# Performance work log

Measured on AMD Instinct MI355X. Metric: run time of the kernel, lower is better.

The kernel has to match this reference:

```python
import jax, jax.numpy as jnp
import numpy as np

N_MET = 100_000
N_RXN = 50_000
E_SUB = 2_000_000
E_ALL = 4_000_000
MSG_DIM = 16
HIDDEN = 32


def setup_inputs() -> dict:
    key = jax.random.key(0)
    ks = jax.random.split(key, 16)
    x_met = jax.random.normal(ks[0], (N_MET,), dtype=jnp.float32)
    sto_sub = jax.random.uniform(ks[1], (E_SUB,), dtype=jnp.float32, minval=0.0, maxval=1.0)
    sto_all = jax.random.normal(ks[2], (E_ALL,), dtype=jnp.float32)
    met_sub = jax.random.randint(ks[3], (E_SUB,), 0, N_MET)
    rxn_sub = jax.random.randint(ks[4], (E_SUB,), 0, N_RXN)
    met_all = jax.random.randint(ks[5], (E_ALL,), 0, N_MET)
    rxn_all = jax.random.randint(ks[6], (E_ALL,), 0, N_RXN)
    # msg_mlp: Linear(2->HIDDEN), Tanh, Linear(HIDDEN->MSG_DIM)
    W1m = jax.random.normal(ks[7], (2, HIDDEN), jnp.float32) / np.sqrt(2.0)
    b1m = jnp.zeros((HIDDEN,), jnp.float32)
    W2m = jax.random.normal(ks[8], (HIDDEN, MSG_DIM), jnp.float32) / np.sqrt(HIDDEN)
    b2m = jnp.zeros((MSG_DIM,), jnp.float32)
    # rate_mlp: Linear(MSG_DIM->HIDDEN), Tanh, Linear(HIDDEN->1)
    W1r = jax.random.normal(ks[9], (MSG_DIM, HIDDEN), jnp.float32) / np.sqrt(MSG_DIM)
    b1r = jnp.zeros((HIDDEN,), jnp.float32)
    W2r = jax.random.normal(ks[10], (HIDDEN, 1), jnp.float32) / np.sqrt(HIDDEN)
    b2r = jnp.zeros((1,), jnp.float32)
    return {
        "x_met": x_met, "sto_sub": sto_sub, "sto_all": sto_all,
        "W1m": W1m, "b1m": b1m, "W2m": W2m, "b2m": b2m,
        "W1r": W1r, "b1r": b1r, "W2r": W2r, "b2r": b2r,
        "met_sub": met_sub, "rxn_sub": rxn_sub,
        "met_all": met_all, "rxn_all": rxn_all,
    }


def reference(x_met, sto_sub, sto_all, W1m, b1m, W2m, b2m, W1r, b1r, W2r, b2r,
              met_sub, rxn_sub, met_all, rxn_all):
    # gather substrate node features and build per-edge MLP input [E_sub, 2]
    msg_in = jnp.stack([x_met[met_sub], sto_sub], axis=-1)
    # msg MLP: tanh hidden, linear out -> [E_sub, MSG_DIM]
    msg = jnp.tanh(msg_in @ W1m + b1m) @ W2m + b2m
    # scatter-add messages into reactions -> [N_RXN, MSG_DIM]
    h_rxn = jax.ops.segment_sum(msg, rxn_sub, num_segments=N_RXN)
    # rate MLP + softplus -> per-reaction rate v [N_RXN]
    v = jax.nn.softplus((jnp.tanh(h_rxn @ W1r + b1r) @ W2r + b2r)[:, 0])
    # stoichiometric contributions scattered into metabolites -> dxdt [N_MET]
    contrib = sto_all * v[rxn_all]
    dxdt = jax.ops.segment_sum(contrib, met_all, num_segments=N_MET)
    return dxdt, v
```

## Files before the change

### kernel.cpp

```cpp
#include <hip/hip_runtime.h>

#define N_MET 100000
#define N_RXN 50000
#define E_SUB 2000000
#define E_ALL 4000000
#define MSG_DIM 16
#define HIDDEN 32

#define NBKT_A 391
#define NB_ALL 245
#define TILE_A 16384
#define LOFFA_W (NBKT_A + 1)
#define NBKT_S 782
#define NB_SUB 245
#define TILE_S 8192


__device__ __forceinline__ float fast_tanh(float x) {
    const float ax = fabsf(x);
    const float e = __expf(2.0f * ax);
    const float t = 1.0f - 2.0f * __builtin_amdgcn_rcpf(e + 1.0f);
    return copysignf(t, x);
}


__global__ __launch_bounds__(1024) void hist_sub_kernel(
    const int* __restrict__ rxn_sub, int* __restrict__ histS)
{
    __shared__ int hb[NBKT_S];
    const int t = threadIdx.x, bk = blockIdx.x;
    for (int i = t; i < NBKT_S; i += 1024) hb[i] = 0;
    __syncthreads();
#pragma unroll
    for (int k = 0; k < 2; ++k) {
        const int i = bk * 2048 + (k << 10) + t;
        if (i < E_SUB / 4) {
            const int4 r = ((const int4*)rxn_sub)[i];
            atomicAdd(&hb[r.x >> 6], 1);
            atomicAdd(&hb[r.y >> 6], 1);
            atomicAdd(&hb[r.z >> 6], 1);
            atomicAdd(&hb[r.w >> 6], 1);
        }
    }
    __syncthreads();
    for (int i = t; i < NBKT_S; i += 1024) histS[bk * NBKT_S + i] = hb[i];
}

__global__ __launch_bounds__(256) void scan_cols_sub_kernel(
    int* __restrict__ histS, int* __restrict__ tot_s)
{
    __shared__ int wsum[4];
    const int b = blockIdx.x;
    const int t = threadIdx.x, lane = t & 63, w = t >> 6;
    const int val = (t < NB_SUB) ? histS[(size_t)t * NBKT_S + b] : 0;
    int x = val;
#pragma unroll
    for (int off = 1; off < 64; off <<= 1) {
        const int y = __shfl_up(x, off);
        if (lane >= off) x += y;
    }
    if (lane == 63) wsum[w] = x;
    __syncthreads();
    if (w == 0) {
        int s = (lane < 4) ? wsum[lane] : 0;
#pragma unroll
        for (int off = 1; off < 4; off <<= 1) {
            const int y = __shfl_up(s, off);
            if (lane >= off) s += y;
        }
        if (lane < 4) wsum[lane] = s;
    }
    __syncthreads();
    const int excl = ((w > 0) ? wsum[w - 1] : 0) + x - val;
    if (t < NB_SUB) histS[(size_t)t * NBKT_S + b] = excl;
    if (t == 0) tot_s[b] = wsum[3];
}

__global__ __launch_bounds__(256) void scan_base_sub_kernel(
    const int* __restrict__ tot_s, int* __restrict__ base_s)
{
    __shared__ int wsum[4];
    const int t = threadIdx.x, lane = t & 63, w = t >> 6;
    int carry = 0;
    for (int basei = 0; basei < NBKT_S; basei += 256) {
        const int i = basei + t;
        const int val = (i < NBKT_S) ? tot_s[i] : 0;
        int x = val;
#pragma unroll
        for (int off = 1; off < 64; off <<= 1) {
            const int y = __shfl_up(x, off);
            if (lane >= off) x += y;
        }
        if (lane == 63) wsum[w] = x;
        __syncthreads();
        if (w == 0) {
            int s = (lane < 4) ? wsum[lane] : 0;
#pragma unroll
            for (int off = 1; off < 4; off <<= 1) {
                const int y = __shfl_up(s, off);
                if (lane >= off) s += y;
            }
            if (lane < 4) wsum[lane] = s;
        }
        __syncthreads();
        const int excl = carry + ((w > 0) ? wsum[w - 1] : 0) + x - val;
        if (i < NBKT_S) base_s[i] = excl;
        carry += wsum[3];
        __syncthreads();
    }
}


__global__ __launch_bounds__(1024) void scatter_bin_sub_kernel(
    const float* __restrict__ x_met, const float* __restrict__ sto_sub,
    const int* __restrict__ met_sub, const int* __restrict__ rxn_sub,
    const int* __restrict__ hist, const int* __restrict__ base,
    float2* __restrict__ pxs)
{
    __shared__ float2 se[TILE_S];
    __shared__ int cnt[NBKT_S];
    __shared__ int loff[NBKT_S + 1];
    __shared__ int goff[NBKT_S];
    const int t = threadIdx.x, bk = blockIdx.x;
    for (int i = t; i < NBKT_S; i += 1024) {
        cnt[i] = 0;
        goff[i] = hist[bk * NBKT_S + i] + base[i];
    }
    __syncthreads();

    const int e0 = bk * TILE_S;
    const int rem = min(TILE_S, E_SUB - e0);
    const int tb = 8 * t;
    float2 pay[8]; int meta[8];
    if (tb + 8 <= rem) {
        const int4 r01 = ((const int4*)(rxn_sub + e0))[2 * t];
        const int4 r23 = ((const int4*)(rxn_sub + e0))[2 * t + 1];
        const int4 m01 = ((const int4*)(met_sub + e0))[2 * t];
        const int4 m23 = ((const int4*)(met_sub + e0))[2 * t + 1];
        const float4 s01 = ((const float4*)(sto_sub + e0))[2 * t];
        const float4 s23 = ((const float4*)(sto_sub + e0))[2 * t + 1];
        const int rr[8] = {r01.x, r01.y, r01.z, r01.w, r23.x, r23.y, r23.z, r23.w};
        const int mm[8] = {m01.x, m01.y, m01.z, m01.w, m23.x, m23.y, m23.z, m23.w};
        const float ss[8] = {s01.x, s01.y, s01.z, s01.w, s23.x, s23.y, s23.z, s23.w};
#pragma unroll
        for (int k = 0; k < 8; ++k) {
            const int r = rr[k];
            const float x = x_met[mm[k]];
            const int sb = (__float_as_int(ss[k]) & ~63) | (r & 63);
            pay[k] = make_float2(x, __int_as_float(sb));
            const int q = r >> 6;
            meta[k] = (atomicAdd(&cnt[q], 1) << 10) | q;
        }
    } else {
#pragma unroll
        for (int k = 0; k < 8; ++k) {
            const int e = e0 + tb + k;
            if (e < E_SUB) {
                const int r = rxn_sub[e];
                const float x = x_met[met_sub[e]];
                const int sb = (__float_as_int(sto_sub[e]) & ~63) | (r & 63);
                pay[k] = make_float2(x, __int_as_float(sb));
                const int q = r >> 6;
                meta[k] = (atomicAdd(&cnt[q], 1) << 10) | q;
            } else meta[k] = -1;
        }
    }
    __syncthreads();

    if (t < 64) {
        int carry = 0;
        for (int bb = 0; bb < NBKT_S; bb += 64) {
            const int idx = bb + t;
            const int val = (idx < NBKT_S) ? cnt[idx] : 0;
            int x = val;
#pragma unroll
            for (int off = 1; off < 64; off <<= 1) {
                const int y = __shfl_up(x, off);
                if (t >= off) x += y;
            }
            if (idx < NBKT_S) loff[idx] = carry + x - val;
            carry += __shfl(x, 63);
        }
        if (t == 0) loff[NBKT_S] = carry;
    }
    __syncthreads();

#pragma unroll
    for (int k = 0; k < 8; ++k) {
        if (meta[k] >= 0)
            se[loff[meta[k] & 1023] + (meta[k] >> 10)] = pay[k];
    }
    __syncthreads();

    const int w = t >> 6, lane = t & 63;
    for (int q = w; q < NBKT_S; q += 16) {
        const int s = loff[q], lenq = loff[q + 1] - s, d = goff[q];
        for (int i = lane; i < lenq; i += 64)
            pxs[d + i] = se[s + i];
    }
}

__global__ __launch_bounds__(512, 6) void bucket_msg_kernel(
    const float2* __restrict__ pxs,
    const int* __restrict__ base, const int* __restrict__ tot,
    const float* __restrict__ W1m, const float* __restrict__ b1m,
    const float* __restrict__ W2m, const float* __restrict__ b2m,
    const float* __restrict__ W1r, const float* __restrict__ b1r,
    const float* __restrict__ W2r, const float* __restrict__ b2r,
    float* __restrict__ v)
{
    __shared__ float2 se[4096];
    __shared__ float  sth[64 * 33];
    __shared__ int    cnt[64];
    __shared__ int    soff[65];
    __shared__ int    ccnt[64];
    __shared__ float  sW2m[HIDDEN * MSG_DIM];
    __shared__ float  sb2m[MSG_DIM];
    __shared__ float  sW1r[MSG_DIM * HIDDEN];
    __shared__ float  sb1r[HIDDEN];
    __shared__ float  sW2r[HIDDEN];
    __shared__ float  sb2r;
    __shared__ float  sh[64 * 17];

    const int t = threadIdx.x;
    const int w = t >> 6, l = t & 63;
    const int half = l >> 5, j = l & 31;

    for (int i = t; i < HIDDEN * MSG_DIM; i += 512) sW2m[i] = W2m[i];
    for (int i = t; i < MSG_DIM * HIDDEN; i += 512) sW1r[i] = W1r[i];
    if (t < MSG_DIM) sb2m[t] = b2m[t];
    if (t < HIDDEN) sb1r[t] = b1r[t];
    if (t >= 64 && t < 64 + HIDDEN) sW2r[t - 64] = W2r[t - 64];
    if (t == 128) sb2r = b2r[0];
    if (t < 64) ccnt[t] = 0;

    const float w1x = W1m[j];
    const float w1y = W1m[HIDDEN + j];
    const float w1b = b1m[j];

    const int b = blockIdx.x;
    const int beg = base[b];
    const int end = beg + tot[b];

    float acc[4] = {0.0f, 0.0f, 0.0f, 0.0f};

    for (int cb = beg; cb < end; cb += 4096) {
        if (t < 64) cnt[t] = 0;
        __syncthreads();

        float2 pay[8];
        int meta[8];
#pragma unroll
        for (int k = 0; k < 8; ++k) {
            const int idx = cb + t + (k << 9);
            if (idx < end) {
                const float2 pv = pxs[idx];
                const int r = __float_as_int(pv.y) & 63;
                meta[k] = (atomicAdd(&cnt[r], 1) << 6) | r;
                pay[k] = pv;
            } else meta[k] = -1;
        }
        __syncthreads();

        if (t < 64) {
            const int orig = cnt[t];
            int x = orig;
#pragma unroll
            for (int off = 1; off < 64; off <<= 1) {
                const int y = __shfl_up(x, off);
                if (t >= off) x += y;
            }
            soff[t] = x - orig;
            if (t == 63) soff[64] = x;
            ccnt[t] += orig;
        }
        __syncthreads();

#pragma unroll
        for (int k = 0; k < 8; ++k) {
            if (meta[k] >= 0)
                se[soff[meta[k] & 63] + (meta[k] >> 6)] = pay[k];
        }
        __syncthreads();

#pragma unroll
        for (int p = 0; p < 4; ++p) {
            const int q = (w << 3) + (p << 1) + half;
            const int rb = soff[q];
            const int rl = soff[q + 1] - rb;
            float a0 = 0.0f, a1 = 0.0f;
            int i = 0;
            for (; i + 2 <= rl; i += 2) {
                const float2 e0 = se[rb + i];
                const float2 e1 = se[rb + i + 1];
                a0 += fast_tanh(fmaf(e0.x, w1x, fmaf(e0.y, w1y, w1b)));
                a1 += fast_tanh(fmaf(e1.x, w1x, fmaf(e1.y, w1y, w1b)));
            }
            if (i < rl) {
                const float2 e0 = se[rb + i];
                a0 += fast_tanh(fmaf(e0.x, w1x, fmaf(e0.y, w1y, w1b)));
            }
            acc[p] += a0 + a1;
        }
        __syncthreads();
    }

#pragma unroll
    for (int p = 0; p < 4; ++p) {
        const int q = (w << 3) + (p << 1) + half;
        sth[q * 33 + j] = acc[p];
    }
    __syncthreads();

    {
        const int r = t & 63, g = (t >> 6) << 1;
        const float cntf = (float)ccnt[r];
        float h0 = cntf * sb2m[g + 0], h1 = cntf * sb2m[g + 1];
#pragma unroll 8
        for (int jj = 0; jj < HIDDEN; ++jj) {
            const float ts = sth[r * 33 + jj];
            h0 = fmaf(ts, sW2m[jj * MSG_DIM + g + 0], h0);
            h1 = fmaf(ts, sW2m[jj * MSG_DIM + g + 1], h1);
        }
        sh[r * 17 + g + 0] = h0;
        sh[r * 17 + g + 1] = h1;
    }
    __syncthreads();

    if (t < 64) {
        const int r = b * 64 + t;
        if (r < N_RXN) {
            float h[MSG_DIM];
#pragma unroll
            for (int d = 0; d < MSG_DIM; ++d) h[d] = sh[t * 17 + d];
            float acc2 = sb2r;
#pragma unroll 2
            for (int jj = 0; jj < HIDDEN; ++jj) {
                float z = sb1r[jj];
#pragma unroll
                for (int d = 0; d < MSG_DIM; ++d)
                    z = fmaf(h[d], sW1r[d * HIDDEN + jj], z);
                acc2 = fmaf(fast_tanh(z), sW2r[jj], acc2);
            }
            v[r] = fmaxf(acc2, 0.0f) + log1pf(expf(-fabsf(acc2)));
        }
    }
}


__global__ __launch_bounds__(1024) void scatter_bin_kernel(
    const float* __restrict__ sto_all, const float* __restrict__ v,
    const int* __restrict__ met_all, const int* __restrict__ rxn_all,
    int* __restrict__ loffA, float* __restrict__ pc)
{
    __shared__ float sp[TILE_A];
    __shared__ int cnt[NBKT_A];
    __shared__ int loff[NBKT_A + 1];
    const int t = threadIdx.x, bk = blockIdx.x;
    for (int i = t; i < NBKT_A; i += 1024) cnt[i] = 0;
    __syncthreads();

    const int e0 = bk * TILE_A;
    const int rem = min(TILE_A, E_ALL - e0);
    const int tb = 16 * t;
    int meta[16];
    const bool full = (tb + 16 <= rem);
    if (full) {
#pragma unroll
        for (int kk = 0; kk < 4; ++kk) {
            const int4 m = ((const int4*)(met_all + e0))[4 * t + kk];
            meta[4 * kk + 0] = (atomicAdd(&cnt[m.x >> 8], 1) << 17) | m.x;
            meta[4 * kk + 1] = (atomicAdd(&cnt[m.y >> 8], 1) << 17) | m.y;
            meta[4 * kk + 2] = (atomicAdd(&cnt[m.z >> 8], 1) << 17) | m.z;
            meta[4 * kk + 3] = (atomicAdd(&cnt[m.w >> 8], 1) << 17) | m.w;
        }
    } else {
#pragma unroll
        for (int k = 0; k < 16; ++k) {
            const int e = e0 + tb + k;
            if (e < E_ALL) {
                const int m = met_all[e];
                meta[k] = (atomicAdd(&cnt[m >> 8], 1) << 17) | m;
            } else meta[k] = -1;
        }
    }
    __syncthreads();

    if (t < 64) {
        int carry = 0;
        for (int bb = 0; bb < NBKT_A; bb += 64) {
            const int idx = bb + t;
            const int val = (idx < NBKT_A) ? cnt[idx] : 0;
            int x = val;
#pragma unroll
            for (int off = 1; off < 64; off <<= 1) {
                const int y = __shfl_up(x, off);
                if (t >= off) x += y;
            }
            if (idx < NBKT_A) loff[idx] = carry + x - val;
            carry += __shfl(x, 63);
        }
        if (t == 0) loff[NBKT_A] = carry;
    }
    __syncthreads();

    if (t < LOFFA_W) loffA[bk * LOFFA_W + t] = loff[t];

    if (full) {
#pragma unroll
        for (int kk = 0; kk < 4; ++kk) {
            const int4 r = ((const int4*)(rxn_all + e0))[4 * t + kk];
            const float4 s = ((const float4*)(sto_all + e0))[4 * t + kk];
            const int rr[4] = {r.x, r.y, r.z, r.w};
            const float ss[4] = {s.x, s.y, s.z, s.w};
#pragma unroll
            for (int u = 0; u < 4; ++u) {
                const int mt = meta[4 * kk + u];
                const int m = mt & 0x1FFFF;
                const float c = ss[u] * v[rr[u]];
                const int cb = (__float_as_int(c) & ~255) | (m & 255);
                sp[loff[m >> 8] + (mt >> 17)] = __int_as_float(cb);
            }
        }
    } else {
#pragma unroll
        for (int k = 0; k < 16; ++k) {
            const int e = e0 + tb + k;
            if (e < E_ALL) {
                const int mt = meta[k];
                const int m = mt & 0x1FFFF;
                const float c = sto_all[e] * v[rxn_all[e]];
                const int cb = (__float_as_int(c) & ~255) | (m & 255);
                sp[loff[m >> 8] + (mt >> 17)] = __int_as_float(cb);
            }
        }
    }
    __syncthreads();

    for (int i = 4 * t; i < rem; i += 4096)
        *(float4*)(pc + e0 + i) = *(const float4*)(sp + i);
}

__global__ __launch_bounds__(512) void bucket_accum_kernel(
    const float* __restrict__ pc, const int* __restrict__ loffA,
    float* __restrict__ dxdt)
{
    __shared__ float acc[256];
    const int q = blockIdx.x, t = threadIdx.x;
    const int w = t >> 6, lane = t & 63;
    if (t < 256) acc[t] = 0.0f;
    __syncthreads();

    const int nt = (NB_ALL - 1 - w) / 8 + 1;
    int sv = 0, ev = 0;
    if (lane < nt) {
        const int tile = w + 8 * lane;
        sv = loffA[tile * LOFFA_W + q];
        ev = loffA[tile * LOFFA_W + q + 1];
    }
    for (int it = 0; it < nt; ++it) {
        const int s = __shfl(sv, it);
        const int e = __shfl(ev, it);
        const int tbase = (w + 8 * it) * TILE_A;
        for (int i = s + lane; i < e; i += 64) {
            const float pv = pc[tbase + i];
            atomicAdd(&acc[__float_as_int(pv) & 255], pv);
        }
    }
    __syncthreads();
    if (t < 256) {
        const int met = q * 256 + t;
        if (met < N_MET) dxdt[met] = acc[t];
    }
}

extern "C" void kernel_launch(void* const* d_in, const int* in_sizes, int n_in,
                              void* d_out, int out_size, void* d_ws, size_t ws_size,
                              hipStream_t stream) {
    const float* x_met   = (const float*)d_in[0];
    const float* sto_sub = (const float*)d_in[1];
    const float* sto_all = (const float*)d_in[2];
    const float* W1m     = (const float*)d_in[3];
    const float* b1m     = (const float*)d_in[4];
    const float* W2m     = (const float*)d_in[5];
    const float* b2m     = (const float*)d_in[6];
    const float* W1r     = (const float*)d_in[7];
    const float* b1r     = (const float*)d_in[8];
    const float* W2r     = (const float*)d_in[9];
    const float* b2r     = (const float*)d_in[10];
    const int*   met_sub = (const int*)d_in[11];
    const int*   rxn_sub = (const int*)d_in[12];
    const int*   met_all = (const int*)d_in[13];
    const int*   rxn_all = (const int*)d_in[14];

    float* dxdt = (float*)d_out;
    float* v    = dxdt + N_MET;

    char* ws = (char*)d_ws;
    int* histS  = (int*)ws;  ws += (((size_t)NB_SUB * NBKT_S * 4 + 15) / 16) * 16;
    int* tot_s  = (int*)ws;  ws += ((sizeof(int) * NBKT_S + 15) / 16) * 16;
    int* base_s = (int*)ws;  ws += ((sizeof(int) * NBKT_S + 15) / 16) * 16;
    int* loffA  = (int*)ws;  ws += (((size_t)NB_ALL * LOFFA_W * 4 + 15) / 16) * 16;
    char* P = ws;
    float2* pxs = (float2*)P;
    float*  pc  = (float*)P;

    hist_sub_kernel<<<NB_SUB, 1024, 0, stream>>>(rxn_sub, histS);
    scan_cols_sub_kernel<<<NBKT_S, 256, 0, stream>>>(histS, tot_s);
    scan_base_sub_kernel<<<1, 256, 0, stream>>>(tot_s, base_s);

    scatter_bin_sub_kernel<<<NB_SUB, 1024, 0, stream>>>(
        x_met, sto_sub, met_sub, rxn_sub, histS, base_s, pxs);
    bucket_msg_kernel<<<NBKT_S, 512, 0, stream>>>(
        pxs, base_s, tot_s, W1m, b1m, W2m, b2m, W1r, b1r, W2r, b2r, v);

    scatter_bin_kernel<<<NB_ALL, 1024, 0, stream>>>(
        sto_all, v, met_all, rxn_all, loffA, pc);
    bucket_accum_kernel<<<NBKT_A, 512, 0, stream>>>(pc, loffA, dxdt);
}
```

Measured before the change: 252.3 us.

## Drop global histogram/scan passes; consumer gathers per-tile bucket segments

Removes the three histogram and scan kernels for the substrate pass. Each scatter block now writes its locally bucket-sorted tile contiguously at its own tile offset and publishes its local bucket offsets. Each bucket block gathers its segments from all 245 tiles into shared memory after a per-block prefix scan. This saves three launches and one read of rxn_sub, at the cost of fragmented gathers of small per-tile segments in the consumer. fast_tanh is also simplified by dropping the abs/copysign, which can overflow to inf for large positive inputs but still gives the right limit through rcp.

After: 250.9 us. Within noise of the previous version (-0.5%).

```diff
diff --git a/kernel.cpp b/kernel.cpp
--- a/kernel.cpp
+++ b/kernel.cpp
@@ -14,118 +14,25 @@
 #define NBKT_S 782
 #define NB_SUB 245
 #define TILE_S 8192
+#define LOFFS_W (NBKT_S + 1)
 
 
 __device__ __forceinline__ float fast_tanh(float x) {
-    const float ax = fabsf(x);
-    const float e = __expf(2.0f * ax);
-    const float t = 1.0f - 2.0f * __builtin_amdgcn_rcpf(e + 1.0f);
-    return copysignf(t, x);
-}
-
-
-__global__ __launch_bounds__(1024) void hist_sub_kernel(
-    const int* __restrict__ rxn_sub, int* __restrict__ histS)
-{
-    __shared__ int hb[NBKT_S];
-    const int t = threadIdx.x, bk = blockIdx.x;
-    for (int i = t; i < NBKT_S; i += 1024) hb[i] = 0;
-    __syncthreads();
-#pragma unroll
-    for (int k = 0; k < 2; ++k) {
-        const int i = bk * 2048 + (k << 10) + t;
-        if (i < E_SUB / 4) {
-            const int4 r = ((const int4*)rxn_sub)[i];
-            atomicAdd(&hb[r.x >> 6], 1);
-            atomicAdd(&hb[r.y >> 6], 1);
-            atomicAdd(&hb[r.z >> 6], 1);
-            atomicAdd(&hb[r.w >> 6], 1);
-        }
-    }
-    __syncthreads();
-    for (int i = t; i < NBKT_S; i += 1024) histS[bk * NBKT_S + i] = hb[i];
-}
-
-__global__ __launch_bounds__(256) void scan_cols_sub_kernel(
-    int* __restrict__ histS, int* __restrict__ tot_s)
-{
-    __shared__ int wsum[4];
-    const int b = blockIdx.x;
-    const int t = threadIdx.x, lane = t & 63, w = t >> 6;
-    const int val = (t < NB_SUB) ? histS[(size_t)t * NBKT_S + b] : 0;
-    int x = val;
-#pragma unroll
-    for (int off = 1; off < 64; off <<= 1) {
-        const int y = __shfl_up(x, off);
-        if (lane >= off) x += y;
-    }
-    if (lane == 63) wsum[w] = x;
-    __syncthreads();
-    if (w == 0) {
-        int s = (lane < 4) ? wsum[lane] : 0;
-#pragma unroll
-        for (int off = 1; off < 4; off <<= 1) {
-            const int y = __shfl_up(s, off);
-            if (lane >= off) s += y;
-        }
-        if (lane < 4) wsum[lane] = s;
-    }
-    __syncthreads();
-    const int excl = ((w > 0) ? wsum[w - 1] : 0) + x - val;
-    if (t < NB_SUB) histS[(size_t)t * NBKT_S + b] = excl;
-    if (t == 0) tot_s[b] = wsum[3];
-}
-
-__global__ __launch_bounds__(256) void scan_base_sub_kernel(
-    const int* __restrict__ tot_s, int* __restrict__ base_s)
-{
-    __shared__ int wsum[4];
-    const int t = threadIdx.x, lane = t & 63, w = t >> 6;
-    int carry = 0;
-    for (int basei = 0; basei < NBKT_S; basei += 256) {
-        const int i = basei + t;
-        const int val = (i < NBKT_S) ? tot_s[i] : 0;
-        int x = val;
-#pragma unroll
-        for (int off = 1; off < 64; off <<= 1) {
-            const int y = __shfl_up(x, off);
-            if (lane >= off) x += y;
-        }
-        if (lane == 63) wsum[w] = x;
-        __syncthreads();
-        if (w == 0) {
-            int s = (lane < 4) ? wsum[lane] : 0;
-#pragma unroll
-            for (int off = 1; off < 4; off <<= 1) {
-                const int y = __shfl_up(s, off);
-                if (lane >= off) s += y;
-            }
-            if (lane < 4) wsum[lane] = s;
-        }
-        __syncthreads();
-        const int excl = carry + ((w > 0) ? wsum[w - 1] : 0) + x - val;
-        if (i < NBKT_S) base_s[i] = excl;
-        carry += wsum[3];
-        __syncthreads();
-    }
+    const float e = __expf(2.0f * x);
+    return 1.0f - 2.0f * __builtin_amdgcn_rcpf(e + 1.0f);
 }
 
 
 __global__ __launch_bounds__(1024) void scatter_bin_sub_kernel(
     const float* __restrict__ x_met, const float* __restrict__ sto_sub,
     const int* __restrict__ met_sub, const int* __restrict__ rxn_sub,
-    const int* __restrict__ hist, const int* __restrict__ base,
-    float2* __restrict__ pxs)
+    int* __restrict__ loffS, float2* __restrict__ pxs)
 {
     __shared__ float2 se[TILE_S];
     __shared__ int cnt[NBKT_S];
     __shared__ int loff[NBKT_S + 1];
-    __shared__ int goff[NBKT_S];
     const int t = threadIdx.x, bk = blockIdx.x;
-    for (int i = t; i < NBKT_S; i += 1024) {
-        cnt[i] = 0;
-        goff[i] = hist[bk * NBKT_S + i] + base[i];
-    }
+    for (int i = t; i < NBKT_S; i += 1024) cnt[i] = 0;
     __syncthreads();
 
     const int e0 = bk * TILE_S;
@@ -190,19 +97,17 @@
         if (meta[k] >= 0)
             se[loff[meta[k] & 1023] + (meta[k] >> 10)] = pay[k];
     }
-    __syncthreads();
-
-    const int w = t >> 6, lane = t & 63;
-    for (int q = w; q < NBKT_S; q += 16) {
-        const int s = loff[q], lenq = loff[q + 1] - s, d = goff[q];
-        for (int i = lane; i < lenq; i += 64)
-            pxs[d + i] = se[s + i];
-    }
+    for (int i = t; i <= NBKT_S; i += 1024) loffS[bk * LOFFS_W + i] = loff[i];
+    __syncthreads();
+
+    const float4* src = (const float4*)se;
+    float4* dst = (float4*)(pxs + (size_t)e0);
+    const int n4 = rem >> 1;
+    for (int i = t; i < n4; i += 1024) dst[i] = src[i];
 }
 
 __global__ __launch_bounds__(512, 6) void bucket_msg_kernel(
-    const float2* __restrict__ pxs,
-    const int* __restrict__ base, const int* __restrict__ tot,
+    const float2* __restrict__ pxs, const int* __restrict__ loffS,
     const float* __restrict__ W1m, const float* __restrict__ b1m,
     const float* __restrict__ W2m, const float* __restrict__ b2m,
     const float* __restrict__ W1r, const float* __restrict__ b1r,
@@ -214,6 +119,8 @@
     __shared__ int    cnt[64];
     __shared__ int    soff[65];
     __shared__ int    ccnt[64];
+    __shared__ int    sbeg[NB_SUB];
+    __shared__ int    spfx[NB_SUB + 1];
     __shared__ float  sW2m[HIDDEN * MSG_DIM];
     __shared__ float  sb2m[MSG_DIM];
     __shared__ float  sW1r[MSG_DIM * HIDDEN];
@@ -225,6 +132,7 @@
     const int t = threadIdx.x;
     const int w = t >> 6, l = t & 63;
     const int half = l >> 5, j = l & 31;
+    const int b = blockIdx.x;
 
     for (int i = t; i < HIDDEN * MSG_DIM; i += 512) sW2m[i] = W2m[i];
     for (int i = t; i < MSG_DIM * HIDDEN; i += 512) sW1r[i] = W1r[i];
@@ -233,28 +141,60 @@
     if (t >= 64 && t < 64 + HIDDEN) sW2r[t - 64] = W2r[t - 64];
     if (t == 128) sb2r = b2r[0];
     if (t < 64) ccnt[t] = 0;
+    if (t < NB_SUB) {
+        const int s0 = loffS[t * LOFFS_W + b];
+        sbeg[t] = s0;
+        spfx[t] = loffS[t * LOFFS_W + b + 1] - s0;
+    }
+    __syncthreads();
+    if (t < 64) {
+        int carry = 0;
+        for (int bb = 0; bb < NB_SUB; bb += 64) {
+            const int idx = bb + t;
+            const int val = (idx < NB_SUB) ? spfx[idx] : 0;
+            int x = val;
+#pragma unroll
+            for (int off = 1; off < 64; off <<= 1) {
+                const int y = __shfl_up(x, off);
+                if (t >= off) x += y;
+            }
+            if (idx < NB_SUB) spfx[idx] = carry + x - val;
+            carry += __shfl(x, 63);
+        }
+        if (t == 0) spfx[NB_SUB] = carry;
+    }
+    __syncthreads();
+    const int T = spfx[NB_SUB];
 
     const float w1x = W1m[j];
     const float w1y = W1m[HIDDEN + j];
     const float w1b = b1m[j];
 
-    const int b = blockIdx.x;
-    const int beg = base[b];
-    const int end = beg + tot[b];
-
     float acc[4] = {0.0f, 0.0f, 0.0f, 0.0f};
 
-    for (int cb = beg; cb < end; cb += 4096) {
+    for (int cb = 0; cb < T; cb += 4096) {
+        const int ce = min(cb + 4096, T);
+        const int clen = ce - cb;
         if (t < 64) cnt[t] = 0;
+
+        for (int tt = w; tt < NB_SUB; tt += 8) {
+            const int s0 = spfx[tt];
+            const int s1 = spfx[tt + 1];
+            const int lo = max(s0, cb), hi = min(s1, ce);
+            const int gb = tt * TILE_S + sbeg[tt] - s0;
+            for (int i = lo + l; i < hi; i += 64)
+                se[i - cb] = pxs[gb + i];
+        }
         __syncthreads();
 
         float2 pay[8];
         int meta[8];
+        const int tb2 = t << 3;
 #pragma unroll
         for (int k = 0; k < 8; ++k) {
-            const int idx = cb + t + (k << 9);
-            if (idx < end) {
-                const float2 pv = pxs[idx];
+            const int slot = tb2 + k;
+            if (slot < clen) {
+                const float2 pv = se[slot];
                 const int r = __float_as_int(pv.y) & 63;
                 meta[k] = (atomicAdd(&cnt[r], 1) << 6) | r;
                 pay[k] = pv;
@@ -497,22 +437,16 @@
     float* v    = dxdt + N_MET;
 
     char* ws = (char*)d_ws;
-    int* histS  = (int*)ws;  ws += (((size_t)NB_SUB * NBKT_S * 4 + 15) / 16) * 16;
-    int* tot_s  = (int*)ws;  ws += ((sizeof(int) * NBKT_S + 15) / 16) * 16;
-    int* base_s = (int*)ws;  ws += ((sizeof(int) * NBKT_S + 15) / 16) * 16;
+    int* loffS  = (int*)ws;  ws += (((size_t)NB_SUB * LOFFS_W * 4 + 15) / 16) * 16;
     int* loffA  = (int*)ws;  ws += (((size_t)NB_ALL * LOFFA_W * 4 + 15) / 16) * 16;
     char* P = ws;
     float2* pxs = (float2*)P;
     float*  pc  = (float*)P;
 
-    hist_sub_kernel<<<NB_SUB, 1024, 0, stream>>>(rxn_sub, histS);
-    scan_cols_sub_kernel<<<NBKT_S, 256, 0, stream>>>(histS, tot_s);
-    scan_base_sub_kernel<<<1, 256, 0, stream>>>(tot_s, base_s);
-
     scatter_bin_sub_kernel<<<NB_SUB, 1024, 0, stream>>>(
-        x_met, sto_sub, met_sub, rxn_sub, histS, base_s, pxs);
+        x_met, sto_sub, met_sub, rxn_sub, loffS, pxs);
     bucket_msg_kernel<<<NBKT_S, 512, 0, stream>>>(
-        pxs, base_s, tot_s, W1m, b1m, W2m, b2m, W1r, b1r, W2r, b2r, v);
+        pxs, loffS, W1m, b1m, W2m, b2m, W1r, b1r, W2r, b2r, v);
 
     scatter_bin_kernel<<<NB_ALL, 1024, 0, stream>>>(
         sto_all, v, met_all, rxn_all, loffA, pc);
```
